# Kernel optimization log

Hardware: AMD Instinct MI355X
Metric: run time of the kernel (lower is better)

## Reference

```python
import jax, jax.numpy as jnp
import numpy as np

N_MEL = 80
PRENET = 256
ENC = 512
ARNN = 1024
DRNN = 1024
ATT = 128
NF = 32
K = 31
B, S, T = 16, 256, 400


def _lstm_cell(x, h, c, Wih, Whh, bih, bhh):
    # torch nn.LSTMCell math: gates ordered i, f, g, o
    z = x @ Wih.T + bih + h @ Whh.T + bhh
    i, f, g, o = jnp.split(z, 4, axis=-1)
    c_new = jax.nn.sigmoid(f) * c + jax.nn.sigmoid(i) * jnp.tanh(g)
    h_new = jax.nn.sigmoid(o) * jnp.tanh(c_new)
    return h_new, c_new


def setup_inputs() -> dict:
    key = jax.random.key(0)
    ks = jax.random.split(key, 24)
    g = lambda i, shape: (jax.random.normal(ks[i], shape, jnp.float32) * 0.02)
    inp = {
        'memory': jax.random.normal(ks[0], (B, S, ENC), jnp.float32),
        'decoder_inputs': jax.random.normal(ks[1], (B, N_MEL, T), jnp.float32),
        # prenet (LinearNorm, no bias in tacotron2 prenet)
        'Wpre1': g(2, (PRENET, N_MEL)),
        'Wpre2': g(3, (PRENET, PRENET)),
        # attention LSTMCell: input = prenet + enc = 256 + 512 = 768
        'Wih_a': g(4, (4 * ARNN, PRENET + ENC)),
        'Whh_a': g(5, (4 * ARNN, ARNN)),
        'bih_a': jnp.zeros((4 * ARNN,), jnp.float32),
        'bhh_a': jnp.zeros((4 * ARNN,), jnp.float32),
        # location-sensitive attention
        'Wq': g(6, (ATT, ARNN)),
        'Wm': g(7, (ATT, ENC)),
        'v': g(8, (ATT,)),
        'Wloc_conv': g(9, (NF, 2, K)),
        'Wloc_dense': g(10, (ATT, NF)),
        # decoder LSTMCell: input = att_rnn + enc = 1024 + 512 = 1536
        'Wih_d': g(11, (4 * DRNN, ARNN + ENC)),
        'Whh_d': g(12, (4 * DRNN, DRNN)),
        'bih_d': jnp.zeros((4 * DRNN,), jnp.float32),
        'bhh_d': jnp.zeros((4 * DRNN,), jnp.float32),
        # projections from [decoder_hidden ; context] = 1536
        'Wproj': g(13, (N_MEL, DRNN + ENC)),
        'bproj': jnp.zeros((N_MEL,), jnp.float32),
        'Wgate': g(14, (1, DRNN + ENC)),
        'bgate': jnp.zeros((1,), jnp.float32),
        'memory_lengths': jax.random.randint(ks[15], (B,), S // 2, S + 1),
    }
    return inp


def reference(memory, decoder_inputs, Wpre1, Wpre2, Wih_a, Whh_a, bih_a, bhh_a,
              Wq, Wm, v, Wloc_conv, Wloc_dense, Wih_d, Whh_d, bih_d, bhh_d,
              Wproj, bproj, Wgate, bgate, memory_lengths):
    # pad mask: True where position is beyond the encoder length
    pad_mask = jnp.arange(S)[None, :] >= memory_lengths[:, None]  # [B,S]
    proc_mem = memory @ Wm.T  # [B,S,ATT], memory_layer precomputed once

    # parse_decoder_inputs + go frame: [B,80,T] -> [T,B,80], prepend zeros
    di = jnp.transpose(decoder_inputs, (2, 0, 1))
    di = jnp.concatenate([jnp.zeros((1, B, N_MEL), di.dtype), di], axis=0)
    # prenet (dropout treated as identity for deterministic reference)
    pre = jax.nn.relu(jax.nn.relu(di @ Wpre1.T) @ Wpre2.T)  # [T+1,B,256]
    xs = pre[:-1]  # loop consumes indices 0..T-1

    carry0 = (jnp.zeros((B, ARNN)), jnp.zeros((B, ARNN)),
              jnp.zeros((B, DRNN)), jnp.zeros((B, DRNN)),
              jnp.zeros((B, S)), jnp.zeros((B, S)), jnp.zeros((B, ENC)))

    def step(carry, x):
        ah, ac, dh, dc, aw, awc, ctx = carry
        ah, ac = _lstm_cell(jnp.concatenate([x, ctx], -1), ah, ac,
                            Wih_a, Whh_a, bih_a, bhh_a)
        # location features from [prev_weights ; cum_weights]
        awcat = jnp.stack([aw, awc], axis=1)  # [B,2,S]
        loc = jax.lax.conv_general_dilated(
            awcat, Wloc_conv, (1,), ((K // 2, K // 2),),
            dimension_numbers=('NCH', 'OIH', 'NCH'))  # [B,NF,S]
        proc_att = jnp.einsum('bfs,af->bsa', loc, Wloc_dense)  # [B,S,ATT]
        q = ah @ Wq.T  # [B,ATT]
        e = jnp.tanh(q[:, None, :] + proc_att + proc_mem) @ v  # [B,S]
        e = jnp.where(pad_mask, -1e9, e)
        aw = jax.nn.softmax(e, axis=-1)
        ctx = jnp.einsum('bs,bse->be', aw, memory)  # [B,ENC]
        awc = awc + aw
        dh, dc = _lstm_cell(jnp.concatenate([ah, ctx], -1), dh, dc,
                            Wih_d, Whh_d, bih_d, bhh_d)
        hac = jnp.concatenate([dh, ctx], -1)  # [B,1536]
        mel = hac @ Wproj.T + bproj  # [B,80]
        gate = (hac @ Wgate.T + bgate)[:, 0]  # [B]
        return (ah, ac, dh, dc, aw, awc, ctx), (mel, gate, aw)

    _, (mels, gates, aligns) = jax.lax.scan(step, carry0, xs)
    mel_outputs = jnp.transpose(mels, (1, 2, 0))  # [B,80,T]
    gate_outputs = gates.T  # [B,T]
    alignments = jnp.transpose(aligns, (1, 0, 2))  # [B,T,S]
    return mel_outputs, gate_outputs, alignments
```

## Files before the change

### kernel.cpp

```cpp
#include <hip/hip_runtime.h>

typedef unsigned short ushort_t;
typedef unsigned int uint_t;
typedef float f32x4_t __attribute__((ext_vector_type(4)));
typedef short bf16x8_t __attribute__((ext_vector_type(8)));

#define NBATCH 16
#define SMEM   256
#define TSTEPS 400

#define F_XSB   0u
#define F_PM    819200u
#define F_MMIX  1343488u
#define F_W1T   1675264u
#define F_W2T   1695744u
#define F_AHB   1761280u
#define F_DHB   1777664u
#define F_CTXB  1794048u
#define F_DHF   1802240u
#define F_AWG   1835008u
#define F_FLG   1851392u
#define ZERO_BASE  F_AHB
#define ZERO_COUNT 95616u
#define F_QP    1856896u

#define AHF  0
#define CTXF 64
#define DHFL 192
#define AWF  320
#define PRF  336

#define A_AH    0
#define A_CTX   32768
#define A_XS    49152
#define A_RED   57344
#define A_QWQ   61440
#define A_QH    69632
#define D_AH    0
#define D_CTX   32768
#define D_DH    49152
#define D_COMB  81920
#define M_LOCU  0
#define M_QSM   20480
#define M_VSM   20992
#define M_ESM   21504
#define M_RED   22528
#define M_SMAW  22784
#define M_SMAWC 23808
#define M_MEM   24832
#define M_PART  155904
#define P_DHP   0
#define P_AWP   65536
#define SMEM_BYTES 160000

struct Ptrs {
  const float *memory, *dec_in, *Wpre1, *Wpre2, *Wih_a, *Whh_a, *bih_a, *bhh_a,
              *Wq, *Wm, *v, *Wc, *Wld, *Wih_d, *Whh_d, *bih_d, *bhh_d,
              *Wproj, *bproj, *Wgate, *bgate;
  const int *mlen;
  float *ws;
  float *out;
};

__device__ __forceinline__ float ftanh(float x) {
  float e = __expf(2.f * x);
  return 1.f - 2.f / (e + 1.f);
}
__device__ __forceinline__ float fsig(float x) { return 1.f / (1.f + __expf(-x)); }

__device__ __forceinline__ unsigned f2bfbits(float x) {
  unsigned u = __builtin_bit_cast(unsigned, x);
  return (u + 0x7FFFu + ((u >> 16) & 1u)) >> 16;
}
__device__ __forceinline__ float bf2f(ushort_t u) {
  unsigned v = ((unsigned)u) << 16;
  return __builtin_bit_cast(float, v);
}
__device__ __forceinline__ bf16x8_t packbf8(const float* f) {
  bf16x8_t r;
#pragma unroll
  for (int j = 0; j < 8; ++j) r[j] = (short)f2bfbits(f[j]);
  return r;
}
__device__ __forceinline__ bf16x8_t pack_from_f4(const float* src) {
  const float4* s4 = (const float4*)src;
  float4 lo = s4[0], hi = s4[1];
  float tmp[8] = {lo.x, lo.y, lo.z, lo.w, hi.x, hi.y, hi.z, hi.w};
  return packbf8(tmp);
}
__device__ __forceinline__ bf16x8_t ldbf8(const ushort_t* p) {
  return *(const bf16x8_t*)p;
}
__device__ __forceinline__ unsigned long long ldull_a(const unsigned long long* p) {
  return __hip_atomic_load(p, __ATOMIC_RELAXED, __HIP_MEMORY_SCOPE_AGENT);
}
__device__ __forceinline__ void stull_a(unsigned long long* p, unsigned long long v) {
  __hip_atomic_store(p, v, __ATOMIC_RELAXED, __HIP_MEMORY_SCOPE_AGENT);
}
__device__ __forceinline__ void stf_a(float* p, float v) {
  __hip_atomic_store(p, v, __ATOMIC_RELAXED, __HIP_MEMORY_SCOPE_AGENT);
}
__device__ __forceinline__ float ldf_a(const float* p) {
  return __hip_atomic_load(p, __ATOMIC_RELAXED, __HIP_MEMORY_SCOPE_AGENT);
}
__device__ __forceinline__ void pollge(int* flg, int slot, int thr) {
  while (__hip_atomic_load(flg + slot * 16, __ATOMIC_RELAXED, __HIP_MEMORY_SCOPE_AGENT) < thr)
    __builtin_amdgcn_s_sleep(1);
}
__device__ __forceinline__ void sig(int* flg, int slot, int val) {
  __hip_atomic_store(flg + slot * 16, val, __ATOMIC_RELAXED, __HIP_MEMORY_SCOPE_AGENT);
}
__device__ __forceinline__ void lds_st8(char* smc, int base, int row, int row_sh,
                                        int bytecol, unsigned long long v) {
  *(unsigned long long*)(smc + base + (row << row_sh) + (bytecol ^ ((row & 7) << 4))) = v;
}
__device__ __forceinline__ bf16x8_t lds_bf8(const char* smc, int base, int row,
                                            int row_sh, int bytecol) {
  return *(const bf16x8_t*)(smc + base + (row << row_sh) + (bytecol ^ ((row & 7) << 4)));
}
#define MFMA16(a,b,c) __builtin_amdgcn_mfma_f32_16x16x32_bf16((a),(b),(c),0,0,0)

__global__ __launch_bounds__(256) void k_zero(Ptrs p) {
  unsigned i = blockIdx.x * 256 + threadIdx.x;
  if (i < ZERO_COUNT) p.ws[ZERO_BASE + i] = 0.f;
}

__global__ __launch_bounds__(256) void k_transpose(Ptrs p) {
  int i = blockIdx.x * 256 + threadIdx.x;
  if (i < 20480) {
    int m = i >> 8, c = i & 255;
    p.ws[F_W1T + i] = p.Wpre1[c * 80 + m];
  } else if (i < 20480 + 65536) {
    int j = i - 20480;
    int pp = j >> 8, q = j & 255;
    p.ws[F_W2T + j] = p.Wpre2[q * 256 + pp];
  }
}

__global__ __launch_bounds__(256) void k_prenet(Ptrs p) {
  __shared__ float dil[NBATCH * 80];
  __shared__ float h1[NBATCH * 256];
  const int t = blockIdx.x, tid = threadIdx.x;
  const float* W1T = p.ws + F_W1T;
  const float* W2T = p.ws + F_W2T;

  for (int i = tid; i < NBATCH * 80; i += 256) {
    int b = i / 80, m = i - b * 80;
    dil[i] = (t == 0) ? 0.f : p.dec_in[((size_t)b * 80 + m) * 400 + (t - 1)];
  }
  __syncthreads();

  float acc[NBATCH];
#pragma unroll
  for (int b = 0; b < NBATCH; ++b) acc[b] = 0.f;
  for (int m = 0; m < 80; ++m) {
    float w = W1T[m * 256 + tid];
#pragma unroll
    for (int b = 0; b < NBATCH; ++b) acc[b] = fmaf(dil[b * 80 + m], w, acc[b]);
  }
#pragma unroll
  for (int b = 0; b < NBATCH; ++b) h1[b * 256 + tid] = fmaxf(acc[b], 0.f);
  __syncthreads();

#pragma unroll
  for (int b = 0; b < NBATCH; ++b) acc[b] = 0.f;
  for (int q = 0; q < 256; ++q) {
    float w = W2T[q * 256 + tid];
#pragma unroll
    for (int b = 0; b < NBATCH; ++b) acc[b] = fmaf(h1[b * 256 + q], w, acc[b]);
  }
  ushort_t* xsbU = (ushort_t*)(p.ws + F_XSB);
#pragma unroll
  for (int b = 0; b < NBATCH; ++b)
    xsbU[((size_t)(t * NBATCH + b)) * 256 + tid] = (ushort_t)f2bfbits(fmaxf(acc[b], 0.f));
}

__global__ __launch_bounds__(256) void k_procmem(Ptrs p) {
  __shared__ alignas(16) float msl[16 * 512];
  const int b = blockIdx.x >> 4, s0 = (blockIdx.x & 15) << 4;
  const int tid = threadIdx.x;
  const float4* src = (const float4*)(p.memory + ((size_t)(b * SMEM + s0)) * 512);
  float4* dst = (float4*)msl;
  for (int i = tid; i < 16 * 512 / 4; i += 256) dst[i] = src[i];
  __syncthreads();

  const int a = tid & 127, sg = tid >> 7;
  const float4* wm = (const float4*)(p.Wm + (size_t)a * 512);
  float* pm = p.ws + F_PM;
  float acc[8];
#pragma unroll
  for (int j = 0; j < 8; ++j) acc[j] = 0.f;
  for (int k = 0; k < 128; ++k) {
    float4 w = wm[k];
#pragma unroll
    for (int j = 0; j < 8; ++j) {
      float4 m = ((const float4*)(msl + (size_t)(sg * 8 + j) * 512))[k];
      acc[j] += w.x * m.x + w.y * m.y + w.z * m.z + w.w * m.w;
    }
  }
#pragma unroll
  for (int j = 0; j < 8; ++j)
    pm[((size_t)(b * SMEM + s0 + sg * 8 + j)) * 128 + a] = acc[j];
}

__global__ __launch_bounds__(512) void k_premix(Ptrs p) {
  const int b = blockIdx.x, tid = threadIdx.x;
  float* M = p.ws + F_MMIX;
  for (int i = tid; i < 81 * 256; i += 512) {
    int row = i >> 8, s = i & 255;
    const float* wrow = (row < 80) ? p.Wproj + (size_t)row * 1536 + 1024 : p.Wgate + 1024;
    const float4* w4 = (const float4*)wrow;
    const float4* m4 = (const float4*)(p.memory + ((size_t)(b * 256 + s)) * 512);
    float acc = 0.f;
#pragma unroll 4
    for (int k = 0; k < 128; ++k) {
      float4 w = w4[k], m = m4[k];
      acc += w.x * m.x + w.y * m.y + w.z * m.z + w.w * m.w;
    }
    M[((size_t)b * 81 + row) * 256 + s] = acc;
  }
}

__global__ __launch_bounds__(512, 1) void k_scan(Ptrs p) {
  extern __shared__ char smc[];
  const int bid = blockIdx.x, tid = threadIdx.x;
  const int wid = tid >> 6, lane = tid & 63;
  const int m16 = lane & 15, kq = lane >> 4;

  float* ws = p.ws;
  ushort_t* xsbU  = (ushort_t*)(ws + F_XSB);
  float*    pmF   = ws + F_PM;
  float*    Mx    = ws + F_MMIX;
  unsigned long long* ahb8 = (unsigned long long*)(ws + F_AHB);
  unsigned long long* dhb8 = (unsigned long long*)(ws + F_DHB);
  unsigned long long* ctxb8 = (unsigned long long*)(ws + F_CTXB);
  float*    dhfF  = ws + F_DHF;
  float*    awGF  = ws + F_AWG;
  float*    qpF   = ws + F_QP;
  int*      flg   = (int*)(ws + F_FLG);
  float* out_mel  = p.out;
  float* out_gate = p.out + 512000;
  float* out_al   = p.out + 518400;

  if (bid < 64) {
    const int ls = wid >> 1, half = wid & 1;
    const int strip = (bid << 2) | ls;
    const int gA = m16 & 3, jA = m16 >> 2;
    const int wrowA = gA * 1024 + strip * 4 + jA;
    bf16x8_t wA[28];
#pragma unroll
    for (int c = 0; c < 28; ++c) {
      int k0 = (half * 28 + c) * 32 + kq * 8;
      const float* src = (k0 < 768) ? p.Wih_a + (size_t)wrowA * 768 + k0
                                    : p.Whh_a + (size_t)wrowA * 1024 + (k0 - 768);
      wA[c] = pack_from_f4(src);
    }
    const int nnA = strip * 4 + kq;
    float biasA[4];
#pragma unroll
    for (int r = 0; r < 4; ++r) biasA[r] = p.bih_a[r * 1024 + nnA] + p.bhh_a[r * 1024 + nnA];
    float acState = 0.f;
    float* ared = (float*)(smc + A_RED);
    float* qwq  = (float*)(smc + A_QWQ);
    float* qh   = (float*)(smc + A_QH);
    for (int i = tid; i < 2048; i += 512) {
      int a = i >> 4, c = i & 15;
      qwq[i] = p.Wq[(size_t)a * 1024 + bid * 16 + c];
    }
    __syncthreads();

    for (int t = 0; t < TSTEPS; ++t) {
      const int pc = t & 1, pp = (t + 1) & 1;
      if (tid < 64) pollge(flg, AHF + tid, t);
      __syncthreads();
      {
        const unsigned long long* ag = ahb8 + (size_t)pp * 4096;
        const unsigned long long* xg = (const unsigned long long*)xsbU + (size_t)t * 1024;
        unsigned long long tA[8], tX[2];
#pragma unroll
        for (int i = 0; i < 8; ++i) tA[i] = ldull_a(ag + tid + i * 512);
#pragma unroll
        for (int i = 0; i < 2; ++i) tX[i] = xg[tid + i * 512];
#pragma unroll
        for (int i = 0; i < 8; ++i) { int u = tid + i * 512; lds_st8(smc, A_AH, u >> 8, 11, (u & 255) * 8, tA[i]); }
#pragma unroll
        for (int i = 0; i < 2; ++i) { int u = tid + i * 512; lds_st8(smc, A_XS, u >> 6, 9, (u & 63) * 8, tX[i]); }
      }
      __syncthreads();
      f32x4_t a0 = {0,0,0,0}, a1 = {0,0,0,0};
      if (half == 0) {
#pragma unroll
        for (int c = 0; c < 8; ++c) {
          bf16x8_t bf = lds_bf8(smc, A_XS, m16, 9, c * 64 + kq * 16);
          if (c & 1) a1 = MFMA16(wA[c], bf, a1); else a0 = MFMA16(wA[c], bf, a0);
        }
#pragma unroll
        for (int c = 24; c < 28; ++c) {
          bf16x8_t bf = lds_bf8(smc, A_AH, m16, 11, (c - 24) * 64 + kq * 16);
          if (c & 1) a1 = MFMA16(wA[c], bf, a1); else a0 = MFMA16(wA[c], bf, a0);
        }
      } else {
#pragma unroll
        for (int c = 0; c < 28; ++c) {
          bf16x8_t bf = lds_bf8(smc, A_AH, m16, 11, (4 + c) * 64 + kq * 16);
          if (c & 1) a1 = MFMA16(wA[c], bf, a1); else a0 = MFMA16(wA[c], bf, a0);
        }
#pragma unroll
        for (int r = 0; r < 4; ++r) ared[((ls * 64 + lane) << 2) + r] = a0[r] + a1[r];
      }
      if (tid < 32) pollge(flg, CTXF + tid, t);
      else if (tid >= 64 && tid < 192) pollge(flg, DHFL + (tid - 64), t - 1);
      __syncthreads();
      {
        const unsigned long long* cg = ctxb8 + (size_t)pp * 2048;
        unsigned long long tC[4];
#pragma unroll
        for (int i = 0; i < 4; ++i) tC[i] = ldull_a(cg + tid + i * 512);
#pragma unroll
        for (int i = 0; i < 4; ++i) { int u = tid + i * 512; lds_st8(smc, A_CTX, u >> 7, 10, (u & 127) * 8, tC[i]); }
      }
      __syncthreads();
      if (half == 0) {
#pragma unroll
        for (int c = 8; c < 24; ++c) {
          bf16x8_t bf = lds_bf8(smc, A_CTX, m16, 10, (c - 8) * 64 + kq * 16);
          if (c & 1) a1 = MFMA16(wA[c], bf, a1); else a0 = MFMA16(wA[c], bf, a0);
        }
        float z[4];
#pragma unroll
        for (int r = 0; r < 4; ++r)
          z[r] = a0[r] + a1[r] + ared[((ls * 64 + lane) << 2) + r] + biasA[r];
        float cn = fsig(z[1]) * acState + fsig(z[0]) * ftanh(z[2]);
        acState = cn;
        float h = fsig(z[3]) * ftanh(cn);
        qh[(m16 << 4) + ls * 4 + kq] = h;
        unsigned hb = f2bfbits(h);
        unsigned b0 = __shfl(hb, m16);
        unsigned b1 = __shfl(hb, m16 + 16);
        unsigned b2 = __shfl(hb, m16 + 32);
        unsigned b3 = __shfl(hb, m16 + 48);
        if (kq == 0) {
          unsigned long long u = (unsigned long long)(b0 | (b1 << 16))
                               | ((unsigned long long)(b2 | (b3 << 16)) << 32);
          stull_a(ahb8 + ((size_t)(pc * 16 + m16)) * 256 + strip, u);
        }
      }
      __syncthreads();
      {
        int a = tid & 127, bg = tid >> 7;
        const float* wrow = qwq + a * 16;
        float s0 = 0.f, s1 = 0.f, s2 = 0.f, s3 = 0.f;
#pragma unroll
        for (int c = 0; c < 16; ++c) {
          float wv = wrow[c];
          s0 = fmaf(wv, qh[((bg * 4 + 0) << 4) + c], s0);
          s1 = fmaf(wv, qh[((bg * 4 + 1) << 4) + c], s1);
          s2 = fmaf(wv, qh[((bg * 4 + 2) << 4) + c], s2);
          s3 = fmaf(wv, qh[((bg * 4 + 3) << 4) + c], s3);
        }
        float* qps = qpF + (size_t)pc * 131072 + bid * 2048 + a;
        stf_a(qps + (size_t)(bg * 4 + 0) * 128, s0);
        stf_a(qps + (size_t)(bg * 4 + 1) * 128, s1);
        stf_a(qps + (size_t)(bg * 4 + 2) * 128, s2);
        stf_a(qps + (size_t)(bg * 4 + 3) * 128, s3);
      }
      __syncthreads();
      if (tid == 0) sig(flg, AHF + bid, t + 1);
    }
  } else if (bid < 192) {
    const int ls = wid >> 2, qt = wid & 3;
    const int strip = ((bid - 64) << 1) | ls;
    const int gD = m16 & 3, jD = m16 >> 2;
    const int wrowD = gD * 1024 + strip * 4 + jD;
    bf16x8_t wD[20];
#pragma unroll
    for (int c = 0; c < 20; ++c) {
      int k0 = (qt * 20 + c) * 32 + kq * 8;
      const float* src = (k0 < 1536) ? p.Wih_d + (size_t)wrowD * 1536 + k0
                                     : p.Whh_d + (size_t)wrowD * 1024 + (k0 - 1536);
      wD[c] = pack_from_f4(src);
    }
    const int nnD = strip * 4 + kq;
    float biasD[4];
#pragma unroll
    for (int r = 0; r < 4; ++r) biasD[r] = p.bih_d[r * 1024 + nnD] + p.bhh_d[r * 1024 + nnD];
    float dcState = 0.f;
    float* comb = (float*)(smc + D_COMB);
    __syncthreads();

    for (int t = 1; t <= TSTEPS; ++t) {
      const int pc = t & 1, pw = (t + 1) & 1;
      if (tid < 32) pollge(flg, CTXF + tid, t);
      else if (tid >= 64 && tid < 192) pollge(flg, DHFL + (tid - 64), t - 1);
      else if (tid >= 192 && tid < 200) pollge(flg, PRF + (tid - 192), t - 2);
      __syncthreads();
      {
        const unsigned long long* ag = ahb8 + (size_t)pw * 4096;
        const unsigned long long* dg = dhb8 + (size_t)pc * 4096;
        unsigned long long tA[8], tD[8];
#pragma unroll
        for (int i = 0; i < 8; ++i) tA[i] = ldull_a(ag + tid + i * 512);
#pragma unroll
        for (int i = 0; i < 8; ++i) tD[i] = ldull_a(dg + tid + i * 512);
#pragma unroll
        for (int i = 0; i < 8; ++i) { int u = tid + i * 512; lds_st8(smc, D_AH, u >> 8, 11, (u & 255) * 8, tA[i]); }
#pragma unroll
        for (int i = 0; i < 8; ++i) { int u = tid + i * 512; lds_st8(smc, D_DH, u >> 8, 11, (u & 255) * 8, tD[i]); }
      }
      {
        const unsigned long long* cg = ctxb8 + (size_t)pw * 2048;
        unsigned long long tC[4];
#pragma unroll
        for (int i = 0; i < 4; ++i) tC[i] = ldull_a(cg + tid + i * 512);
#pragma unroll
        for (int i = 0; i < 4; ++i) { int u = tid + i * 512; lds_st8(smc, D_CTX, u >> 7, 10, (u & 127) * 8, tC[i]); }
      }
      __syncthreads();

      f32x4_t a0 = {0,0,0,0}, a1 = {0,0,0,0};
#define DFRAG_AH(ch)  lds_bf8(smc, D_AH,  m16, 11, (ch) * 64 + kq * 16)
#define DFRAG_CTX(ch) lds_bf8(smc, D_CTX, m16, 10, (ch) * 64 + kq * 16)
#define DFRAG_DH(ch)  lds_bf8(smc, D_DH,  m16, 11, (ch) * 64 + kq * 16)
#define DMFMA(BF) { bf16x8_t bf = (BF); \
        if (c & 1) a1 = MFMA16(wD[c], bf, a1); else a0 = MFMA16(wD[c], bf, a0); }
      if (qt == 0) {
#pragma unroll
        for (int c = 0; c < 20; ++c) DMFMA(DFRAG_AH(c))
      } else if (qt == 1) {
#pragma unroll
        for (int c = 0; c < 20; ++c) { if (c < 12) DMFMA(DFRAG_AH(20 + c)) else DMFMA(DFRAG_CTX(c - 12)) }
      } else if (qt == 2) {
#pragma unroll
        for (int c = 0; c < 20; ++c) { if (c < 8) DMFMA(DFRAG_CTX(8 + c)) else DMFMA(DFRAG_DH(c - 8)) }
      } else {
#pragma unroll
        for (int c = 0; c < 20; ++c) DMFMA(DFRAG_DH(12 + c))
      }
#undef DMFMA
      if (qt != 0) {
#pragma unroll
        for (int r = 0; r < 4; ++r)
          comb[(((ls * 3 + qt - 1) * 64 + lane) << 2) + r] = a0[r] + a1[r];
      }
      __syncthreads();
      if (qt == 0) {
        float z[4];
#pragma unroll
        for (int r = 0; r < 4; ++r) {
          z[r] = a0[r] + a1[r] + biasD[r];
#pragma unroll
          for (int j = 0; j < 3; ++j) z[r] += comb[(((ls * 3 + j) * 64 + lane) << 2) + r];
        }
        float cn = fsig(z[1]) * dcState + fsig(z[0]) * ftanh(z[2]);
        dcState = cn;
        float h = fsig(z[3]) * ftanh(cn);
        stf_a(dhfF + (size_t)pw * 16384 + m16 * 1024 + nnD, h);
        unsigned hb = f2bfbits(h);
        unsigned b0 = __shfl(hb, m16);
        unsigned b1 = __shfl(hb, m16 + 16);
        unsigned b2 = __shfl(hb, m16 + 32);
        unsigned b3 = __shfl(hb, m16 + 48);
        if (kq == 0) {
          unsigned long long u = (unsigned long long)(b0 | (b1 << 16))
                               | ((unsigned long long)(b2 | (b3 << 16)) << 32);
          stull_a(dhb8 + ((size_t)(pw * 16 + m16)) * 256 + strip, u);
        }
      }
      __syncthreads();
      if (tid == 0) sig(flg, DHFL + (bid - 64), t);
    }
  } else if (bid < 224) {
    const int cbid = bid - 192;
    const int b = cbid >> 1, h2 = cbid & 1;
    const int mlenb = p.mlen[b];
    ushort_t* locu = (ushort_t*)(smc + M_LOCU);
    float* qsm   = (float*)(smc + M_QSM);
    float* vsm   = (float*)(smc + M_VSM);
    float* esm   = (float*)(smc + M_ESM);
    float* red   = (float*)(smc + M_RED);
    float* smaw  = (float*)(smc + M_SMAW);
    float* smawc = (float*)(smc + M_SMAWC);
    ushort_t* memu2 = (ushort_t*)(smc + M_MEM);
    float* part  = (float*)(smc + M_PART);
    float* qred  = part;

    bf16x8_t wLd[8];
#pragma unroll
    for (int at = 0; at < 8; ++at)
      wLd[at] = pack_from_f4(p.Wld + ((size_t)(at * 16 + m16)) * 32 + kq * 8);
    bf16x8_t wC[2][2];
#pragma unroll
    for (int ft = 0; ft < 2; ++ft)
#pragma unroll
      for (int ck = 0; ck < 2; ++ck) {
        float tmp[8];
#pragma unroll
        for (int jj = 0; jj < 8; ++jj) {
          int k2 = ck * 32 + kq * 8 + jj;
          float vv = 0.f;
          if (k2 < 62) { int ch = (k2 < 31) ? 0 : 1; int k = k2 - 31 * ch;
            vv = p.Wc[((size_t)(ft * 16 + m16) * 2 + ch) * 31 + k]; }
          tmp[jj] = vv;
        }
        wC[ft][ck] = packbf8(tmp);
      }
    uint_t pmreg[2][8][2];
#pragma unroll
    for (int u = 0; u < 2; ++u) {
      int sloc = (wid * 2 + u) * 16 + m16;
#pragma unroll
      for (int at = 0; at < 8; ++at)
#pragma unroll
        for (int rp = 0; rp < 2; ++rp) {
          const float* src = pmF + ((size_t)(b * 256 + sloc)) * 128 + at * 16 + kq * 4 + rp * 2;
          pmreg[u][at][rp] = f2bfbits(src[0]) | (f2bfbits(src[1]) << 16);
        }
    }
    for (int i = tid; i < 16384; i += 512) {
      int s = i >> 6, c4 = i & 63;
      float4 m = *(const float4*)(p.memory + ((size_t)(b * 256 + s)) * 512 + h2 * 256 + c4 * 4);
      ushort_t* dst = memu2 + s * 256 + c4 * 4;
      dst[0] = (ushort_t)f2bfbits(m.x);
      dst[1] = (ushort_t)f2bfbits(m.y);
      dst[2] = (ushort_t)f2bfbits(m.z);
      dst[3] = (ushort_t)f2bfbits(m.w);
    }
    if (tid < 128) vsm[tid] = p.v[tid];
    if (tid < 256) { smaw[tid] = 0.f; smawc[tid] = 0.f; }
    __syncthreads();

    for (int t = 0; t < TSTEPS; ++t) {
      const int pc = t & 1;
#pragma unroll
      for (int u = 0; u < 4; ++u) {
        int task = wid * 4 + u;
        int stile = task >> 1, ft = task & 1;
        int scol = stile * 16 + m16;
        f32x4_t acc = {0,0,0,0};
#pragma unroll
        for (int ck = 0; ck < 2; ++ck) {
          float tmp[8];
#pragma unroll
          for (int jj = 0; jj < 8; ++jj) {
            int k2 = ck * 32 + kq * 8 + jj;
            float vv = 0.f;
            if (k2 < 62) {
              int ch = (k2 < 31) ? 0 : 1; int k = k2 - 31 * ch;
              int sp = scol + k - 15;
              if (sp >= 0 && sp < 256) vv = (ch ? smawc : smaw)[sp];
            }
            tmp[jj] = vv;
          }
          acc = MFMA16(wC[ft][ck], packbf8(tmp), acc);
        }
#pragma unroll
        for (int r = 0; r < 4; ++r)
          locu[scol * 40 + ft * 16 + kq * 4 + r] = (ushort_t)f2bfbits(acc[r]);
      }
      if (tid < 64) pollge(flg, AHF + tid, t + 1);
      else if (tid < 192) pollge(flg, DHFL + (tid - 64), t - 1);
      else if (tid < 200) pollge(flg, PRF + (tid - 192), t - 3);
      __syncthreads();
      {
        int a2 = (tid & 63) * 2, g = tid >> 6;
        const unsigned long long* qps =
            (const unsigned long long*)(qpF + (size_t)(t & 1) * 131072 + b * 128 + a2);
        float sx = 0.f, sy = 0.f;
#pragma unroll
        for (int j = 0; j < 8; ++j) {
          unsigned long long uv = ldull_a(qps + (size_t)(g * 8 + j) * 1024);
          float2 f = __builtin_bit_cast(float2, uv);
          sx += f.x; sy += f.y;
        }
        qred[g * 128 + a2] = sx;
        qred[g * 128 + a2 + 1] = sy;
      }
      __syncthreads();
      if (tid < 128) {
        float s = 0.f;
#pragma unroll
        for (int g = 0; g < 8; ++g) s += qred[g * 128 + tid];
        qsm[tid] = s;
      }
      __syncthreads();
#pragma unroll
      for (int u = 0; u < 2; ++u) {
        int sloc = (wid * 2 + u) * 16 + m16;
        bf16x8_t Bfrag = ldbf8(locu + sloc * 40 + kq * 8);
        float eacc = 0.f;
#pragma unroll
        for (int at = 0; at < 8; ++at) {
          f32x4_t C = {0,0,0,0};
          C = MFMA16(wLd[at], Bfrag, C);
#pragma unroll
          for (int r = 0; r < 4; ++r) {
            int a = at * 16 + kq * 4 + r;
            uint_t pw_ = pmreg[u][at][r >> 1];
            float pmv = bf2f((ushort_t)((r & 1) ? (pw_ >> 16) : (pw_ & 0xFFFF)));
            eacc = fmaf(vsm[a], ftanh(C[r] + qsm[a] + pmv), eacc);
          }
        }
        eacc += __shfl_xor(eacc, 16);
        eacc += __shfl_xor(eacc, 32);
        if (sloc >= mlenb) eacc = -1.0e9f;
        if (kq == 0) esm[sloc] = eacc;
      }
      __syncthreads();
      float ev = 0.f;
      if (tid < 256) {
        ev = esm[tid];
        float mv = ev;
        for (int o = 32; o; o >>= 1) mv = fmaxf(mv, __shfl_xor(mv, o));
        if (lane == 0) red[wid] = mv;
      }
      __syncthreads();
      float gmax = fmaxf(fmaxf(red[0], red[1]), fmaxf(red[2], red[3]));
      float pv = 0.f;
      if (tid < 256) {
        pv = __expf(ev - gmax);
        float sv = pv;
        for (int o = 32; o; o >>= 1) sv += __shfl_xor(sv, o);
        if (lane == 0) red[8 + wid] = sv;
      }
      __syncthreads();
      float gsum = red[8] + red[9] + red[10] + red[11];
      float awv = 0.f;
      if (tid < 256) {
        awv = pv / gsum;
        smaw[tid] = awv;
        smawc[tid] += awv;
        if (h2 == 0) stf_a(awGF + (size_t)(t & 3) * 4096 + b * 256 + tid, awv);
      }
      __syncthreads();
      {
        const int c = tid & 127, sg = tid >> 7;
        const uint_t* mrow = (const uint_t*)memu2;
        float c0 = 0.f, c1 = 0.f;
#pragma unroll 8
        for (int si = 0; si < 64; ++si) {
          int s = sg * 64 + si;
          uint_t mm = mrow[s * 128 + c];
          float av = smaw[s];
          c0 = fmaf(bf2f((ushort_t)(mm & 0xFFFF)), av, c0);
          c1 = fmaf(bf2f((ushort_t)(mm >> 16)), av, c1);
        }
        part[sg * 256 + c * 2] = c0;
        part[sg * 256 + c * 2 + 1] = c1;
      }
      __syncthreads();
      if (tid < 64) {
        unsigned pk[4];
#pragma unroll
        for (int j = 0; j < 4; ++j) {
          int col = tid * 4 + j;
          float v = part[col] + part[256 + col] + part[512 + col] + part[768 + col];
          pk[j] = f2bfbits(v);
        }
        unsigned long long u = (unsigned long long)(pk[0] | (pk[1] << 16))
                             | ((unsigned long long)(pk[2] | (pk[3] << 16)) << 32);
        stull_a(ctxb8 + ((size_t)(pc * 16 + b)) * 128 + h2 * 64 + tid, u);
      }
      __syncthreads();
      if (tid == 0) {
        sig(flg, CTXF + cbid, t + 1);
        if (h2 == 0) sig(flg, AWF + b, t + 1);
      }
      if (h2 == 0 && tid < 256) out_al[((size_t)b * 400 + t) * 256 + tid] = awv;
    }
  } else if (bid < 232) {
    const int wv = (bid - 224) * 8 + wid;
    int rows[2] = {wv * 2, wv * 2 + 1};
    float wdh[2][16], mreg[2][16][4], biasr[2];
#pragma unroll
    for (int rr = 0; rr < 2; ++rr) {
      int row = rows[rr];
      biasr[rr] = 0.f;
#pragma unroll
      for (int j = 0; j < 16; ++j) wdh[rr][j] = 0.f;
#pragma unroll
      for (int b2 = 0; b2 < 16; ++b2)
#pragma unroll
        for (int j = 0; j < 4; ++j) mreg[rr][b2][j] = 0.f;
      if (row <= 80) {
        const float* wsrc = (row < 80) ? p.Wproj + (size_t)row * 1536 : p.Wgate;
#pragma unroll
        for (int j = 0; j < 16; ++j) wdh[rr][j] = wsrc[lane + 64 * j];
        biasr[rr] = (row < 80) ? p.bproj[row] : p.bgate[0];
#pragma unroll
        for (int b2 = 0; b2 < 16; ++b2)
#pragma unroll
          for (int j = 0; j < 4; ++j)
            mreg[rr][b2][j] = Mx[((size_t)b2 * 81 + row) * 256 + lane + 64 * j];
      }
    }
    float* dhp = (float*)(smc + P_DHP);
    float* awp = (float*)(smc + P_AWP);
    __syncthreads();
    for (int t = 1; t <= TSTEPS; ++t) {
      const int pw = (t + 1) & 1;
      if (tid < 128) pollge(flg, DHFL + tid, t);
      else if (tid < 144) pollge(flg, AWF + tid - 128, t);
      __syncthreads();
      {
        const unsigned long long* ag = (const unsigned long long*)(awGF + (size_t)((t - 1) & 3) * 4096);
        const unsigned long long* dg = (const unsigned long long*)(dhfF + (size_t)pw * 16384);
        unsigned long long tw[4], td[16];
#pragma unroll
        for (int i = 0; i < 4; ++i) tw[i] = ldull_a(ag + tid + i * 512);
#pragma unroll
        for (int i = 0; i < 16; ++i) td[i] = ldull_a(dg + tid + i * 512);
#pragma unroll
        for (int i = 0; i < 4; ++i) ((unsigned long long*)awp)[tid + i * 512] = tw[i];
#pragma unroll
        for (int i = 0; i < 16; ++i) ((unsigned long long*)dhp)[tid + i * 512] = td[i];
      }
      __syncthreads();
      if (wv <= 40) {
        for (int b2 = 0; b2 < 16; ++b2) {
          float h[16];
#pragma unroll
          for (int j = 0; j < 16; ++j) h[j] = dhp[b2 * 1024 + lane + 64 * j];
#pragma unroll
          for (int rr = 0; rr < 2; ++rr) {
            if (rows[rr] > 80) continue;
            float d = 0.f;
#pragma unroll
            for (int j = 0; j < 16; ++j) d = fmaf(wdh[rr][j], h[j], d);
#pragma unroll
            for (int j = 0; j < 4; ++j) d = fmaf(mreg[rr][b2][j], awp[b2 * 256 + lane + 64 * j], d);
            for (int o = 32; o; o >>= 1) d += __shfl_xor(d, o);
            if (lane == 0) {
              d += biasr[rr];
              if (rows[rr] < 80) out_mel[((size_t)b2 * 80 + rows[rr]) * 400 + (t - 1)] = d;
              else out_gate[(size_t)b2 * 400 + (t - 1)] = d;
            }
          }
        }
      }
      __syncthreads();
      if (tid == 0) sig(flg, PRF + (bid - 224), t);
    }
  }
}

extern "C" void kernel_launch(void* const* d_in, const int* in_sizes, int n_in,
                              void* d_out, int out_size, void* d_ws, size_t ws_size,
                              hipStream_t stream) {
  (void)in_sizes; (void)n_in; (void)out_size; (void)ws_size;
  Ptrs p;
  p.memory = (const float*)d_in[0];
  p.dec_in = (const float*)d_in[1];
  p.Wpre1  = (const float*)d_in[2];
  p.Wpre2  = (const float*)d_in[3];
  p.Wih_a  = (const float*)d_in[4];
  p.Whh_a  = (const float*)d_in[5];
  p.bih_a  = (const float*)d_in[6];
  p.bhh_a  = (const float*)d_in[7];
  p.Wq     = (const float*)d_in[8];
  p.Wm     = (const float*)d_in[9];
  p.v      = (const float*)d_in[10];
  p.Wc     = (const float*)d_in[11];
  p.Wld    = (const float*)d_in[12];
  p.Wih_d  = (const float*)d_in[13];
  p.Whh_d  = (const float*)d_in[14];
  p.bih_d  = (const float*)d_in[15];
  p.bhh_d  = (const float*)d_in[16];
  p.Wproj  = (const float*)d_in[17];
  p.bproj  = (const float*)d_in[18];
  p.Wgate  = (const float*)d_in[19];
  p.bgate  = (const float*)d_in[20];
  p.mlen   = (const int*)d_in[21];
  p.ws  = (float*)d_ws;
  p.out = (float*)d_out;

  static bool attr_done = false;
  if (!attr_done) {
    hipFuncSetAttribute((const void*)k_scan,
                        hipFuncAttributeMaxDynamicSharedMemorySize, SMEM_BYTES);
    attr_done = true;
  }

  hipLaunchKernelGGL(k_zero,      dim3((ZERO_COUNT + 255) / 256), dim3(256), 0, stream, p);
  hipLaunchKernelGGL(k_transpose, dim3(336), dim3(256), 0, stream, p);
  hipLaunchKernelGGL(k_prenet,    dim3(400), dim3(256), 0, stream, p);
  hipLaunchKernelGGL(k_procmem,   dim3(256), dim3(256), 0, stream, p);
  hipLaunchKernelGGL(k_premix,    dim3(16),  dim3(512), 0, stream, p);
  hipLaunchKernelGGL(k_scan,      dim3(232), dim3(512), SMEM_BYTES, stream, p);
}
```

Baseline: 7.730 ms.

## Replicate sync flags across four copies and back off polling on slack waits

Each signal flag is now written to four replicated slots, and each block polls the copy chosen by its block index mod 4. This spreads spin-polling traffic from many blocks across more cache lines, so fewer pollers contend on one line. Waits that are expected to have slack now use a longer sleep between polls to cut memory traffic. The query partial-sum compute is also re-indexed so each thread writes two packed 64-bit stores instead of four scalar stores. The cost is extra flag stores per signal, a larger zeroed workspace, and possibly slower wakeup on the backed-off waits.

```diff
diff --git a/kernel.cpp b/kernel.cpp
--- a/kernel.cpp
+++ b/kernel.cpp
@@ -21,14 +21,15 @@
 #define F_AWG   1835008u
 #define F_FLG   1851392u
 #define ZERO_BASE  F_AHB
-#define ZERO_COUNT 95616u
-#define F_QP    1856896u
+#define ZERO_COUNT 112128u
+#define F_QP    1873408u
 
 #define AHF  0
 #define CTXF 64
 #define DHFL 192
 #define AWF  320
 #define PRF  336
+#define FREP 344
 
 #define A_AH    0
 #define A_CTX   32768
@@ -103,12 +104,21 @@
 __device__ __forceinline__ float ldf_a(const float* p) {
   return __hip_atomic_load(p, __ATOMIC_RELAXED, __HIP_MEMORY_SCOPE_AGENT);
 }
-__device__ __forceinline__ void pollge(int* flg, int slot, int thr) {
-  while (__hip_atomic_load(flg + slot * 16, __ATOMIC_RELAXED, __HIP_MEMORY_SCOPE_AGENT) < thr)
+__device__ __forceinline__ void pollge(int* flg, int slot, int thr, int rep) {
+  while (__hip_atomic_load(flg + (slot + rep * FREP) * 16, __ATOMIC_RELAXED,
+                           __HIP_MEMORY_SCOPE_AGENT) < thr)
     __builtin_amdgcn_s_sleep(1);
 }
+__device__ __forceinline__ void pollge_bk(int* flg, int slot, int thr, int rep) {
+  while (__hip_atomic_load(flg + (slot + rep * FREP) * 16, __ATOMIC_RELAXED,
+                           __HIP_MEMORY_SCOPE_AGENT) < thr)
+    __builtin_amdgcn_s_sleep(8);
+}
 __device__ __forceinline__ void sig(int* flg, int slot, int val) {
-  __hip_atomic_store(flg + slot * 16, val, __ATOMIC_RELAXED, __HIP_MEMORY_SCOPE_AGENT);
+#pragma unroll
+  for (int r = 0; r < 4; ++r)
+    __hip_atomic_store(flg + (slot + r * FREP) * 16, val, __ATOMIC_RELAXED,
+                       __HIP_MEMORY_SCOPE_AGENT);
 }
 __device__ __forceinline__ void lds_st8(char* smc, int base, int row, int row_sh,
                                         int bytecol, unsigned long long v) {
@@ -226,6 +236,7 @@
   const int bid = blockIdx.x, tid = threadIdx.x;
   const int wid = tid >> 6, lane = tid & 63;
   const int m16 = lane & 15, kq = lane >> 4;
+  const int rep = bid & 3;
 
   float* ws = p.ws;
   ushort_t* xsbU  = (ushort_t*)(ws + F_XSB);
@@ -271,7 +282,7 @@
 
     for (int t = 0; t < TSTEPS; ++t) {
       const int pc = t & 1, pp = (t + 1) & 1;
-      if (tid < 64) pollge(flg, AHF + tid, t);
+      if (tid < 64) pollge(flg, AHF + tid, t, rep);
       __syncthreads();
       {
         const unsigned long long* ag = ahb8 + (size_t)pp * 4096;
@@ -308,8 +319,8 @@
 #pragma unroll
         for (int r = 0; r < 4; ++r) ared[((ls * 64 + lane) << 2) + r] = a0[r] + a1[r];
       }
-      if (tid < 32) pollge(flg, CTXF + tid, t);
-      else if (tid >= 64 && tid < 192) pollge(flg, DHFL + (tid - 64), t - 1);
+      if (tid < 32) pollge(flg, CTXF + tid, t, rep);
+      else if (tid >= 64 && tid < 192) pollge(flg, DHFL + (tid - 64), t - 1, rep);
       __syncthreads();
       {
         const unsigned long long* cg = ctxb8 + (size_t)pp * 2048;
@@ -347,22 +358,25 @@
       }
       __syncthreads();
       {
-        int a = tid & 127, bg = tid >> 7;
-        const float* wrow = qwq + a * 16;
+        int b = tid & 15, ag = tid >> 4;
+        const float* hrow = qh + b * 16;
         float s0 = 0.f, s1 = 0.f, s2 = 0.f, s3 = 0.f;
 #pragma unroll
         for (int c = 0; c < 16; ++c) {
-          float wv = wrow[c];
-          s0 = fmaf(wv, qh[((bg * 4 + 0) << 4) + c], s0);
-          s1 = fmaf(wv, qh[((bg * 4 + 1) << 4) + c], s1);
-          s2 = fmaf(wv, qh[((bg * 4 + 2) << 4) + c], s2);
-          s3 = fmaf(wv, qh[((bg * 4 + 3) << 4) + c], s3);
-        }
-        float* qps = qpF + (size_t)pc * 131072 + bid * 2048 + a;
-        stf_a(qps + (size_t)(bg * 4 + 0) * 128, s0);
-        stf_a(qps + (size_t)(bg * 4 + 1) * 128, s1);
-        stf_a(qps + (size_t)(bg * 4 + 2) * 128, s2);
-        stf_a(qps + (size_t)(bg * 4 + 3) * 128, s3);
+          float hv = hrow[c];
+          s0 = fmaf(qwq[(ag * 4 + 0) * 16 + c], hv, s0);
+          s1 = fmaf(qwq[(ag * 4 + 1) * 16 + c], hv, s1);
+          s2 = fmaf(qwq[(ag * 4 + 2) * 16 + c], hv, s2);
+          s3 = fmaf(qwq[(ag * 4 + 3) * 16 + c], hv, s3);
+        }
+        unsigned long long u0 = (unsigned long long)__builtin_bit_cast(unsigned, s0)
+                              | ((unsigned long long)__builtin_bit_cast(unsigned, s1) << 32);
+        unsigned long long u1 = (unsigned long long)__builtin_bit_cast(unsigned, s2)
+                              | ((unsigned long long)__builtin_bit_cast(unsigned, s3) << 32);
+        unsigned long long* qps =
+            (unsigned long long*)(qpF + (size_t)pc * 131072 + bid * 2048 + b * 128 + ag * 4);
+        stull_a(qps, u0);
+        stull_a(qps + 1, u1);
       }
       __syncthreads();
       if (tid == 0) sig(flg, AHF + bid, t + 1);
@@ -390,9 +404,9 @@
 
     for (int t = 1; t <= TSTEPS; ++t) {
       const int pc = t & 1, pw = (t + 1) & 1;
-      if (tid < 32) pollge(flg, CTXF + tid, t);
-      else if (tid >= 64 && tid < 192) pollge(flg, DHFL + (tid - 64), t - 1);
-      else if (tid >= 192 && tid < 200) pollge(flg, PRF + (tid - 192), t - 2);
+      if (tid < 32) pollge_bk(flg, CTXF + tid, t, rep);
+      else if (tid >= 64 && tid < 192) pollge(flg, DHFL + (tid - 64), t - 1, rep);
+      else if (tid >= 192 && tid < 200) pollge(flg, PRF + (tid - 192), t - 2, rep);
       __syncthreads();
       {
         const unsigned long long* ag = ahb8 + (size_t)pw * 4096;
@@ -557,9 +571,9 @@
         for (int r = 0; r < 4; ++r)
           locu[scol * 40 + ft * 16 + kq * 4 + r] = (ushort_t)f2bfbits(acc[r]);
       }
-      if (tid < 64) pollge(flg, AHF + tid, t + 1);
-      else if (tid < 192) pollge(flg, DHFL + (tid - 64), t - 1);
-      else if (tid < 200) pollge(flg, PRF + (tid - 192), t - 3);
+      if (tid < 64) pollge(flg, AHF + tid, t + 1, rep);
+      else if (tid < 192) pollge(flg, DHFL + (tid - 64), t - 1, rep);
+      else if (tid < 200) pollge(flg, PRF + (tid - 192), t - 3, rep);
       __syncthreads();
       {
         int a2 = (tid & 63) * 2, g = tid >> 6;
@@ -698,8 +712,8 @@
     __syncthreads();
     for (int t = 1; t <= TSTEPS; ++t) {
       const int pw = (t + 1) & 1;
-      if (tid < 128) pollge(flg, DHFL + tid, t);
-      else if (tid < 144) pollge(flg, AWF + tid - 128, t);
+      if (tid < 128) pollge_bk(flg, DHFL + tid, t, rep);
+      else if (tid < 144) pollge_bk(flg, AWF + tid - 128, t, rep);
       __syncthreads();
       {
         const unsigned long long* ag = (const unsigned long long*)(awGF + (size_t)((t - 1) & 3) * 4096);
```

Result: no change. 7.722 ms (-0.1%).
